# Kernel optimization log

Hardware: AMD Instinct MI355X
Metric: run time of the kernel (lower is better)

The kernel has to match this reference:

```python
import jax, jax.numpy as jnp
import numpy as np

NUM_ITEMS = 10000
EMBED_DIM = 64
USER_PERSPECTIVE_IMPORTANCE = 0.5
LEAKY_SLOPE = 0.2
BATCH = 32
MAX_HIST = 200


def setup_inputs() -> dict:
    key = jax.random.key(0)
    k_ids, k_len, k_items, k_user, k_w, k_b = jax.random.split(key, 6)
    batch_history_ids = jax.random.randint(k_ids, (BATCH, MAX_HIST), 0, NUM_ITEMS, dtype=jnp.int32)
    # lengths must be >= 1 to avoid all-masked softmax rows
    batch_history_lengths = jnp.maximum(
        jax.random.randint(k_len, (BATCH,), 0, MAX_HIST, dtype=jnp.int32), 1)
    items_embedding = jax.random.normal(k_items, (NUM_ITEMS, EMBED_DIM), dtype=jnp.float32)
    user_embedding = jax.random.normal(k_user, (1, EMBED_DIM), dtype=jnp.float32)
    fc_weight = jax.random.normal(k_w, (EMBED_DIM, EMBED_DIM), dtype=jnp.float32) * (1.0 / np.sqrt(EMBED_DIM))
    fc_bias = jax.random.normal(k_b, (EMBED_DIM,), dtype=jnp.float32) * 0.01
    return {
        'batch_history_ids': batch_history_ids,
        'batch_history_lengths': batch_history_lengths,
        'items_embedding': items_embedding,
        'user_embedding': user_embedding,
        'fc_weight': fc_weight,
        'fc_bias': fc_bias,
    }


def reference(batch_history_ids, batch_history_lengths, items_embedding, user_embedding, fc_weight, fc_bias):
    # valid[b, n] = n < length[b]
    valid = jnp.arange(MAX_HIST)[None, :] < batch_history_lengths[:, None]  # [B, N]

    hist_emb = items_embedding[batch_history_ids]  # [B, N, F] ragged gather (padded)

    # item-perspective attention: [B, I, N]
    item_att = jnp.einsum('if,bnf->bin', items_embedding, hist_emb)
    # original adds -inf mask then leaky_relu; leaky_relu(-inf) = -inf -> softmax weight 0
    item_att = jnp.where(valid[:, None, :], jax.nn.leaky_relu(item_att, LEAKY_SLOPE), -jnp.inf)
    item_scores = jax.nn.softmax(item_att, axis=-1)  # [B, I, N]

    # user-perspective attention: constant across the item-query axis (q=1, repeated over I),
    # so compute once as [B, N] and broadcast (same math as 'qif,bnf->bqin').
    user_att = jnp.einsum('f,bnf->bn', user_embedding[0], hist_emb)
    user_att = jnp.where(valid, jax.nn.leaky_relu(user_att, LEAKY_SLOPE), -jnp.inf)
    user_scores = jax.nn.softmax(user_att, axis=-1)  # [B, N]

    w = USER_PERSPECTIVE_IMPORTANCE
    attn = (1.0 - w) * item_scores + w * user_scores[:, None, :]  # [B, I, N]

    personalized = jnp.einsum('bin,bnf->bif', attn, hist_emb)  # [B, I, F]
    projected = personalized @ fc_weight.T + fc_bias  # [B, I, F]
    # final per-item score: dot with item embedding
    return jnp.einsum('bif,if->bi', projected, items_embedding)  # [B, I]
```

## Files before the change

### kernel.cpp

```cpp
#include <hip/hip_runtime.h>
#include <hip/hip_bf16.h>
#include <math.h>

#define NUM_ITEMS 10000
#define EMBED_DIM 64
#define MAX_HIST 200
#define NPAD 208
#define BATCH 32
#define LEAKY 0.2f
#define W_USER 0.5f
#define LOG2E 1.4426950408889634f
#define ECLAMP 110.0f
#define NWTI 157

typedef short bf16x8 __attribute__((ext_vector_type(8)));
typedef float f32x4 __attribute__((ext_vector_type(4)));

__device__ __forceinline__ unsigned short f2bf(float f) {
    __hip_bfloat16 h = __float2bfloat16(f);
    return __builtin_bit_cast(unsigned short, h);
}

__device__ __forceinline__ float bf2f(unsigned short u) {
    return __builtin_bit_cast(float, (unsigned int)u << 16);
}

__device__ __forceinline__ float fexp2(float x) {
#if __has_builtin(__builtin_amdgcn_exp2f)
    return __builtin_amdgcn_exp2f(x);
#else
    return exp2f(x);
#endif
}

__global__ __launch_bounds__(256) void prep_kernel(const int* __restrict__ ids,
                                                   const int* __restrict__ lens,
                                                   const float* __restrict__ items,
                                                   const float* __restrict__ user,
                                                   const float* __restrict__ W,
                                                   const float* __restrict__ bias,
                                                   unsigned short* __restrict__ items_att_bf,
                                                   unsigned short* __restrict__ wti_bf,
                                                   float* __restrict__ bdot,
                                                   unsigned short* __restrict__ hist_bf,
                                                   unsigned short* __restrict__ uh_bf) {
    const int tid = threadIdx.x;
    __shared__ __align__(16) char sbuf[NPAD * EMBED_DIM * 2];
    __shared__ float red[8];
    __shared__ float sh_usf[NPAD];
    __shared__ float sh_uh[4][EMBED_DIM];

    if (blockIdx.x < NWTI) {
        float* shW = (float*)sbuf;
        for (int idx = tid; idx < EMBED_DIM * EMBED_DIM; idx += 256) shW[idx] = W[idx];
        __syncthreads();

        const int g = tid & 63;
        const int isub = tid >> 6;
        const int base = blockIdx.x * 64 + isub * 16;

        for (int k = 0; k < 16; ++k) {
            const int i = base + k;
            if (i >= NUM_ITEMS) break;
            const float* irow = items + (size_t)i * EMBED_DIM;

            float acc = 0.f;
#pragma unroll
            for (int f = 0; f < EMBED_DIM; ++f) acc += irow[f] * shW[f * EMBED_DIM + g];

            wti_bf[i * EMBED_DIM + g] = f2bf(acc);
            items_att_bf[i * EMBED_DIM + g] = f2bf(irow[g] * LOG2E);

            float bv = bias[g] * irow[g];
#pragma unroll
            for (int o = 32; o > 0; o >>= 1) bv += __shfl_xor(bv, o, 64);
            if (g == 0) bdot[i] = bv;
        }
    } else {
        const int b = blockIdx.x - NWTI;
        unsigned short* sh_h = (unsigned short*)sbuf;

        for (int idx = tid; idx < NPAD * 8; idx += 256) {
            const int n = idx >> 3, q = idx & 7;
            bf16x8 v = (bf16x8)0;
            if (n < MAX_HIST) {
                const int id = ids[b * MAX_HIST + n];
                const float4* p = (const float4*)(items + id * EMBED_DIM + q * 8);
                float4 v0 = p[0], v1 = p[1];
                v[0] = (short)f2bf(v0.x); v[1] = (short)f2bf(v0.y);
                v[2] = (short)f2bf(v0.z); v[3] = (short)f2bf(v0.w);
                v[4] = (short)f2bf(v1.x); v[5] = (short)f2bf(v1.y);
                v[6] = (short)f2bf(v1.z); v[7] = (short)f2bf(v1.w);
            }
            *(bf16x8*)(hist_bf + (size_t)(b * NPAD + n) * EMBED_DIM + q * 8) = v;
            *(bf16x8*)(sh_h + (size_t)n * EMBED_DIM + q * 8) = v;
        }

        const int len = lens[b];
        float s = -INFINITY;
        if (tid < len) {
            const int id = ids[b * MAX_HIST + tid];
            const float* h = items + id * EMBED_DIM;
            float a0 = 0.f, a1 = 0.f;
#pragma unroll
            for (int f = 0; f < EMBED_DIM; f += 2) {
                a0 += user[f] * h[f];
                a1 += user[f + 1] * h[f + 1];
            }
            float a = a0 + a1;
            s = fmaxf(a, LEAKY * a);
        }
        float m = s;
#pragma unroll
        for (int o = 32; o > 0; o >>= 1) m = fmaxf(m, __shfl_xor(m, o, 64));
        if ((tid & 63) == 0) red[tid >> 6] = m;
        __syncthreads();
        m = fmaxf(fmaxf(red[0], red[1]), fmaxf(red[2], red[3]));

        float e = (tid < len) ? __expf(s - m) : 0.f;
        float t = e;
#pragma unroll
        for (int o = 32; o > 0; o >>= 1) t += __shfl_xor(t, o, 64);
        if ((tid & 63) == 0) red[4 + (tid >> 6)] = t;
        __syncthreads();
        const float sum = red[4] + red[5] + red[6] + red[7];

        if (tid < NPAD) sh_usf[tid] = (tid < len) ? (e / sum) : 0.f;
        __syncthreads();

        const int f = tid & 63;
        const int part = tid >> 6;
        float uhp = 0.f;
        for (int n = part; n < len; n += 4)
            uhp += sh_usf[n] * bf2f(sh_h[n * EMBED_DIM + f]);
        sh_uh[part][f] = uhp;
        __syncthreads();
        if (tid < EMBED_DIM)
            uh_bf[b * EMBED_DIM + tid] =
                f2bf(sh_uh[0][tid] + sh_uh[1][tid] + sh_uh[2][tid] + sh_uh[3][tid]);
    }
}

__global__ __launch_bounds__(256) void main_kernel(const unsigned short* __restrict__ items_att_bf,
                                                   const unsigned short* __restrict__ wti_bf,
                                                   const float* __restrict__ bdot,
                                                   const unsigned short* __restrict__ hist_bf,
                                                   const unsigned short* __restrict__ uh_bf,
                                                   const int* __restrict__ lens,
                                                   float* __restrict__ out) {
    const int b = blockIdx.y;
    const int tid = threadIdx.x;
    const int lane = tid & 63;
    const int w = tid >> 6;

    __shared__ __align__(16) unsigned short sh_hist[NPAD * EMBED_DIM];

    const int len = lens[b];
    const int ntiles = (len + 15) >> 4;

    const int c16 = lane & 15;
    const int g = lane >> 4;

    bf16x8 u0 = *(const bf16x8*)(uh_bf + b * 64 + g * 8);
    bf16x8 u1 = *(const bf16x8*)(uh_bf + b * 64 + 32 + g * 8);

    const float4* src = (const float4*)(hist_bf + (size_t)b * NPAD * EMBED_DIM);
    const int nf4 = ntiles * 16 * 8;
    for (int c = tid; c < nf4; c += 256) {
        const int n = c >> 3, q = c & 7;
        float4 v = src[c];
        const int byte = (n * 128 + q * 16) ^ ((n & 7) << 4);
        *(float4*)((char*)sh_hist + byte) = v;
    }
    __syncthreads();

    const char* hbase = (const char*)sh_hist;

#define LDA(T, X0, X1)                                                   \
    {                                                                    \
        const int n_ = (T) * 16 + c16;                                   \
        const int base_ = n_ * 128, sw_ = (n_ & 7) << 4;                 \
        X0 = *(const bf16x8*)(hbase + ((base_ + g * 16) ^ sw_));         \
        X1 = *(const bf16x8*)(hbase + ((base_ + 64 + g * 16) ^ sw_));    \
    }

#define EPI(S, H, Se, Sh, MASKED, NB)                                    \
    {                                                                    \
        float s0 = fminf(fmaxf(S[0], LEAKY * S[0]), ECLAMP);             \
        float s1 = fminf(fmaxf(S[1], LEAKY * S[1]), ECLAMP);             \
        float s2 = fminf(fmaxf(S[2], LEAKY * S[2]), ECLAMP);             \
        float s3 = fminf(fmaxf(S[3], LEAKY * S[3]), ECLAMP);             \
        if (MASKED) {                                                    \
            s0 = ((NB) + 0 < len) ? s0 : -INFINITY;                      \
            s1 = ((NB) + 1 < len) ? s1 : -INFINITY;                      \
            s2 = ((NB) + 2 < len) ? s2 : -INFINITY;                      \
            s3 = ((NB) + 3 < len) ? s3 : -INFINITY;                      \
        }                                                                \
        const float e0 = fexp2(s0), e1 = fexp2(s1);                      \
        const float e2 = fexp2(s2), e3 = fexp2(s3);                      \
        Se += (e0 + e1) + (e2 + e3);                                     \
        Sh = fmaf(e0, H[0], fmaf(e1, H[1], fmaf(e2, H[2], fmaf(e3, H[3], Sh)))); \
    }

    const int wbase = blockIdx.x * 256 + w * 16;

    int ild = min(wbase + c16, NUM_ITEMS - 1);
    bf16x8 itc0 = *(const bf16x8*)(items_att_bf + (size_t)ild * 64 + g * 8);
    bf16x8 itc1 = *(const bf16x8*)(items_att_bf + (size_t)ild * 64 + 32 + g * 8);
    bf16x8 wtc0 = *(const bf16x8*)(wti_bf + (size_t)ild * 64 + g * 8);
    bf16x8 wtc1 = *(const bf16x8*)(wti_bf + (size_t)ild * 64 + 32 + g * 8);

#pragma unroll
    for (int it = 0; it < 4; ++it) {
        const int gstart = wbase + it * 64;
        if (gstart >= NUM_ITEMS) break;

        bf16x8 nt0, nt1, nw0, nw1;
        if (it < 3) {
            const int inx = min(wbase + (it + 1) * 64 + c16, NUM_ITEMS - 1);
            nt0 = *(const bf16x8*)(items_att_bf + (size_t)inx * 64 + g * 8);
            nt1 = *(const bf16x8*)(items_att_bf + (size_t)inx * 64 + 32 + g * 8);
            nw0 = *(const bf16x8*)(wti_bf + (size_t)inx * 64 + g * 8);
            nw1 = *(const bf16x8*)(wti_bf + (size_t)inx * 64 + 32 + g * 8);
        }

        f32x4 suf = (f32x4)0.f;
        suf = __builtin_amdgcn_mfma_f32_16x16x32_bf16(u0, wtc0, suf, 0, 0, 0);
        suf = __builtin_amdgcn_mfma_f32_16x16x32_bf16(u1, wtc1, suf, 0, 0, 0);
        const float Su = suf[0];

        float Se = 0.f, Sh = 0.f;
        bf16x8 a0, a1;
        LDA(0, a0, a1)

        for (int t = 0; t < ntiles - 1; ++t) {
            f32x4 S = (f32x4)0.f, H = (f32x4)0.f;
            S = __builtin_amdgcn_mfma_f32_16x16x32_bf16(a0, itc0, S, 0, 0, 0);
            S = __builtin_amdgcn_mfma_f32_16x16x32_bf16(a1, itc1, S, 0, 0, 0);
            H = __builtin_amdgcn_mfma_f32_16x16x32_bf16(a0, wtc0, H, 0, 0, 0);
            H = __builtin_amdgcn_mfma_f32_16x16x32_bf16(a1, wtc1, H, 0, 0, 0);
            bf16x8 p0, p1;
            LDA(t + 1, p0, p1)
            EPI(S, H, Se, Sh, 0, 0)
            a0 = p0; a1 = p1;
        }
        {
            f32x4 S = (f32x4)0.f, H = (f32x4)0.f;
            S = __builtin_amdgcn_mfma_f32_16x16x32_bf16(a0, itc0, S, 0, 0, 0);
            S = __builtin_amdgcn_mfma_f32_16x16x32_bf16(a1, itc1, S, 0, 0, 0);
            H = __builtin_amdgcn_mfma_f32_16x16x32_bf16(a0, wtc0, H, 0, 0, 0);
            H = __builtin_amdgcn_mfma_f32_16x16x32_bf16(a1, wtc1, H, 0, 0, 0);
            const int nb = (ntiles - 1) * 16 + g * 4;
            EPI(S, H, Se, Sh, 1, nb)
        }

        Se += __shfl_xor(Se, 16, 64); Se += __shfl_xor(Se, 32, 64);
        Sh += __shfl_xor(Sh, 16, 64); Sh += __shfl_xor(Sh, 32, 64);

        if (g == 0) {
            const int i = gstart + c16;
            out[(size_t)b * NUM_ITEMS + i] =
                (1.0f - W_USER) * (Sh / Se) + W_USER * Su + bdot[i];
        }

        if (it < 3) { itc0 = nt0; itc1 = nt1; wtc0 = nw0; wtc1 = nw1; }
    }
#undef EPI
#undef LDA
}

extern "C" void kernel_launch(void* const* d_in, const int* in_sizes, int n_in,
                              void* d_out, int out_size, void* d_ws, size_t ws_size,
                              hipStream_t stream) {
    const int* ids = (const int*)d_in[0];
    const int* lens = (const int*)d_in[1];
    const float* items = (const float*)d_in[2];
    const float* user = (const float*)d_in[3];
    const float* W = (const float*)d_in[4];
    const float* bias = (const float*)d_in[5];
    float* out = (float*)d_out;

    char* p = (char*)d_ws;
    unsigned short* items_att_bf = (unsigned short*)p; p += (size_t)NUM_ITEMS * EMBED_DIM * 2;
    unsigned short* wti_bf       = (unsigned short*)p; p += (size_t)NUM_ITEMS * EMBED_DIM * 2;
    float* bdot                  = (float*)p;          p += (size_t)NUM_ITEMS * 4;
    unsigned short* hist_bf      = (unsigned short*)p; p += (size_t)BATCH * NPAD * EMBED_DIM * 2;
    unsigned short* uh_bf        = (unsigned short*)p; p += (size_t)BATCH * EMBED_DIM * 2;

    prep_kernel<<<NWTI + BATCH, 256, 0, stream>>>(ids, lens, items, user, W, bias,
                                                  items_att_bf, wti_bf, bdot,
                                                  hist_bf, uh_bf);

    dim3 grid((NUM_ITEMS + 255) / 256, BATCH);
    main_kernel<<<grid, 256, 0, stream>>>(items_att_bf, wti_bf, bdot, hist_bf, uh_bf, lens, out);
}
```

Measured before the change: 44.58 us.

## Apply FC weight to history side instead of items, using plain bf16 item cast

Reassociates the math so the fc_weight projection is applied to the per-batch history embeddings (histW = hist·Wᵀ, computed with MFMA in the prep kernel) and the log2e scale is folded into a second history copy. The user term and bias are also folded into a per-batch vector v, so the items side needs only a single bf16 cast. The main kernel then streams one item operand instead of two and drops the bdot lookup, at the cost of staging two history tiles in LDS and writing twice the history data in prep. The 64x64 per-item matvec in prep becomes a simple elementwise cast.

```diff
diff --git a/kernel.cpp b/kernel.cpp
--- a/kernel.cpp
+++ b/kernel.cpp
@@ -11,7 +11,7 @@
 #define W_USER 0.5f
 #define LOG2E 1.4426950408889634f
 #define ECLAMP 110.0f
-#define NWTI 157
+#define NCAST 313
 
 typedef short bf16x8 __attribute__((ext_vector_type(8)));
 typedef float f32x4 __attribute__((ext_vector_type(4)));
@@ -33,119 +33,148 @@
 #endif
 }
 
+__device__ __forceinline__ bf16x8 cvt8(float4 a, float4 b) {
+    bf16x8 v;
+    v[0] = (short)f2bf(a.x); v[1] = (short)f2bf(a.y);
+    v[2] = (short)f2bf(a.z); v[3] = (short)f2bf(a.w);
+    v[4] = (short)f2bf(b.x); v[5] = (short)f2bf(b.y);
+    v[6] = (short)f2bf(b.z); v[7] = (short)f2bf(b.w);
+    return v;
+}
+
 __global__ __launch_bounds__(256) void prep_kernel(const int* __restrict__ ids,
                                                    const int* __restrict__ lens,
                                                    const float* __restrict__ items,
                                                    const float* __restrict__ user,
                                                    const float* __restrict__ W,
                                                    const float* __restrict__ bias,
-                                                   unsigned short* __restrict__ items_att_bf,
-                                                   unsigned short* __restrict__ wti_bf,
-                                                   float* __restrict__ bdot,
-                                                   unsigned short* __restrict__ hist_bf,
-                                                   unsigned short* __restrict__ uh_bf) {
+                                                   unsigned short* __restrict__ items_bf,
+                                                   unsigned short* __restrict__ histL_bf,
+                                                   unsigned short* __restrict__ histW_bf,
+                                                   unsigned short* __restrict__ v_bf) {
     const int tid = threadIdx.x;
-    __shared__ __align__(16) char sbuf[NPAD * EMBED_DIM * 2];
+
+    if (blockIdx.x < NCAST) {
+        const int c = blockIdx.x * 256 + tid;
+        if (c < NUM_ITEMS * EMBED_DIM / 8) {
+            const float4* p = (const float4*)items + 2 * c;
+            *(bf16x8*)(items_bf + (size_t)c * 8) = cvt8(p[0], p[1]);
+        }
+        return;
+    }
+
+    const int b = blockIdx.x - NCAST;
+    __shared__ __align__(16) unsigned short sh_h[NPAD * EMBED_DIM];
     __shared__ float red[8];
     __shared__ float sh_usf[NPAD];
     __shared__ float sh_uh[4][EMBED_DIM];
-
-    if (blockIdx.x < NWTI) {
-        float* shW = (float*)sbuf;
-        for (int idx = tid; idx < EMBED_DIM * EMBED_DIM; idx += 256) shW[idx] = W[idx];
-        __syncthreads();
-
-        const int g = tid & 63;
-        const int isub = tid >> 6;
-        const int base = blockIdx.x * 64 + isub * 16;
-
-        for (int k = 0; k < 16; ++k) {
-            const int i = base + k;
-            if (i >= NUM_ITEMS) break;
-            const float* irow = items + (size_t)i * EMBED_DIM;
-
-            float acc = 0.f;
-#pragma unroll
-            for (int f = 0; f < EMBED_DIM; ++f) acc += irow[f] * shW[f * EMBED_DIM + g];
-
-            wti_bf[i * EMBED_DIM + g] = f2bf(acc);
-            items_att_bf[i * EMBED_DIM + g] = f2bf(irow[g] * LOG2E);
-
-            float bv = bias[g] * irow[g];
-#pragma unroll
-            for (int o = 32; o > 0; o >>= 1) bv += __shfl_xor(bv, o, 64);
-            if (g == 0) bdot[i] = bv;
-        }
-    } else {
-        const int b = blockIdx.x - NWTI;
-        unsigned short* sh_h = (unsigned short*)sbuf;
-
-        for (int idx = tid; idx < NPAD * 8; idx += 256) {
-            const int n = idx >> 3, q = idx & 7;
-            bf16x8 v = (bf16x8)0;
-            if (n < MAX_HIST) {
-                const int id = ids[b * MAX_HIST + n];
-                const float4* p = (const float4*)(items + id * EMBED_DIM + q * 8);
-                float4 v0 = p[0], v1 = p[1];
-                v[0] = (short)f2bf(v0.x); v[1] = (short)f2bf(v0.y);
-                v[2] = (short)f2bf(v0.z); v[3] = (short)f2bf(v0.w);
-                v[4] = (short)f2bf(v1.x); v[5] = (short)f2bf(v1.y);
-                v[6] = (short)f2bf(v1.z); v[7] = (short)f2bf(v1.w);
+    __shared__ float sh_uhf[EMBED_DIM];
+
+    const int len = lens[b];
+    const int ntiles = (len + 15) >> 4;
+
+    for (int idx = tid; idx < NPAD * 8; idx += 256) {
+        const int n = idx >> 3;
+        bf16x8 vu = (bf16x8)0, vs = (bf16x8)0;
+        if (n < MAX_HIST) {
+            const int id = ids[b * MAX_HIST + n];
+            const float4* p = (const float4*)(items + (size_t)id * EMBED_DIM + (idx & 7) * 8);
+            float4 v0 = p[0], v1 = p[1];
+            vu = cvt8(v0, v1);
+            float4 s0 = make_float4(v0.x * LOG2E, v0.y * LOG2E, v0.z * LOG2E, v0.w * LOG2E);
+            float4 s1 = make_float4(v1.x * LOG2E, v1.y * LOG2E, v1.z * LOG2E, v1.w * LOG2E);
+            vs = cvt8(s0, s1);
+        }
+        *(bf16x8*)(sh_h + (size_t)idx * 8) = vu;
+        *(bf16x8*)(histL_bf + (size_t)b * NPAD * EMBED_DIM + (size_t)idx * 8) = vs;
+    }
+    __syncthreads();
+
+    {
+        const int lane = tid & 63;
+        const int w = tid >> 6;
+        const int c16 = lane & 15;
+        const int g = lane >> 4;
+        const int f = w * 16 + c16;
+        const float* wrow = W + (size_t)f * EMBED_DIM;
+        float4 wa = *(const float4*)(wrow + g * 8);
+        float4 wb = *(const float4*)(wrow + g * 8 + 4);
+        float4 wc = *(const float4*)(wrow + 32 + g * 8);
+        float4 wd = *(const float4*)(wrow + 32 + g * 8 + 4);
+        bf16x8 b0 = cvt8(wa, wb), b1 = cvt8(wc, wd);
+
+        for (int t = 0; t < ntiles; ++t) {
+            const int n = t * 16 + c16;
+            bf16x8 a0 = *(const bf16x8*)(sh_h + n * EMBED_DIM + g * 8);
+            bf16x8 a1 = *(const bf16x8*)(sh_h + n * EMBED_DIM + 32 + g * 8);
+            f32x4 D = (f32x4)0.f;
+            D = __builtin_amdgcn_mfma_f32_16x16x32_bf16(a0, b0, D, 0, 0, 0);
+            D = __builtin_amdgcn_mfma_f32_16x16x32_bf16(a1, b1, D, 0, 0, 0);
+#pragma unroll
+            for (int j = 0; j < 4; ++j) {
+                const int nr = t * 16 + g * 4 + j;
+                histW_bf[(size_t)(b * NPAD + nr) * EMBED_DIM + f] = f2bf(D[j]);
             }
-            *(bf16x8*)(hist_bf + (size_t)(b * NPAD + n) * EMBED_DIM + q * 8) = v;
-            *(bf16x8*)(sh_h + (size_t)n * EMBED_DIM + q * 8) = v;
-        }
-
-        const int len = lens[b];
-        float s = -INFINITY;
-        if (tid < len) {
-            const int id = ids[b * MAX_HIST + tid];
-            const float* h = items + id * EMBED_DIM;
-            float a0 = 0.f, a1 = 0.f;
-#pragma unroll
-            for (int f = 0; f < EMBED_DIM; f += 2) {
-                a0 += user[f] * h[f];
-                a1 += user[f + 1] * h[f + 1];
-            }
-            float a = a0 + a1;
-            s = fmaxf(a, LEAKY * a);
-        }
-        float m = s;
-#pragma unroll
-        for (int o = 32; o > 0; o >>= 1) m = fmaxf(m, __shfl_xor(m, o, 64));
-        if ((tid & 63) == 0) red[tid >> 6] = m;
-        __syncthreads();
-        m = fmaxf(fmaxf(red[0], red[1]), fmaxf(red[2], red[3]));
-
-        float e = (tid < len) ? __expf(s - m) : 0.f;
-        float t = e;
-#pragma unroll
-        for (int o = 32; o > 0; o >>= 1) t += __shfl_xor(t, o, 64);
-        if ((tid & 63) == 0) red[4 + (tid >> 6)] = t;
-        __syncthreads();
-        const float sum = red[4] + red[5] + red[6] + red[7];
-
-        if (tid < NPAD) sh_usf[tid] = (tid < len) ? (e / sum) : 0.f;
-        __syncthreads();
-
+        }
+    }
+
+    float s = -INFINITY;
+    if (tid < len) {
+        const int id = ids[b * MAX_HIST + tid];
+        const float* h = items + (size_t)id * EMBED_DIM;
+        float a0 = 0.f, a1 = 0.f;
+#pragma unroll
+        for (int fi = 0; fi < EMBED_DIM; fi += 2) {
+            a0 += user[fi] * h[fi];
+            a1 += user[fi + 1] * h[fi + 1];
+        }
+        float a = a0 + a1;
+        s = fmaxf(a, LEAKY * a);
+    }
+    float m = s;
+#pragma unroll
+    for (int o = 32; o > 0; o >>= 1) m = fmaxf(m, __shfl_xor(m, o, 64));
+    if ((tid & 63) == 0) red[tid >> 6] = m;
+    __syncthreads();
+    m = fmaxf(fmaxf(red[0], red[1]), fmaxf(red[2], red[3]));
+
+    float e = (tid < len) ? __expf(s - m) : 0.f;
+    float t = e;
+#pragma unroll
+    for (int o = 32; o > 0; o >>= 1) t += __shfl_xor(t, o, 64);
+    if ((tid & 63) == 0) red[4 + (tid >> 6)] = t;
+    __syncthreads();
+    const float sum = red[4] + red[5] + red[6] + red[7];
+
+    if (tid < NPAD) sh_usf[tid] = (tid < len) ? (e / sum) : 0.f;
+    __syncthreads();
+
+    {
         const int f = tid & 63;
         const int part = tid >> 6;
         float uhp = 0.f;
         for (int n = part; n < len; n += 4)
             uhp += sh_usf[n] * bf2f(sh_h[n * EMBED_DIM + f]);
         sh_uh[part][f] = uhp;
-        __syncthreads();
-        if (tid < EMBED_DIM)
-            uh_bf[b * EMBED_DIM + tid] =
-                f2bf(sh_uh[0][tid] + sh_uh[1][tid] + sh_uh[2][tid] + sh_uh[3][tid]);
-    }
-}
-
-__global__ __launch_bounds__(256) void main_kernel(const unsigned short* __restrict__ items_att_bf,
-                                                   const unsigned short* __restrict__ wti_bf,
-                                                   const float* __restrict__ bdot,
-                                                   const unsigned short* __restrict__ hist_bf,
-                                                   const unsigned short* __restrict__ uh_bf,
+    }
+    __syncthreads();
+    if (tid < EMBED_DIM)
+        sh_uhf[tid] = sh_uh[0][tid] + sh_uh[1][tid] + sh_uh[2][tid] + sh_uh[3][tid];
+    __syncthreads();
+
+    if (tid < EMBED_DIM) {
+        const float* wrow = W + (size_t)tid * EMBED_DIM;
+        float acc = 0.f;
+#pragma unroll 8
+        for (int g2 = 0; g2 < EMBED_DIM; ++g2) acc += sh_uhf[g2] * wrow[g2];
+        v_bf[b * EMBED_DIM + tid] = f2bf(W_USER * acc + bias[tid]);
+    }
+}
+
+__global__ __launch_bounds__(256) void main_kernel(const unsigned short* __restrict__ items_bf,
+                                                   const unsigned short* __restrict__ histL_bf,
+                                                   const unsigned short* __restrict__ histW_bf,
+                                                   const unsigned short* __restrict__ v_bf,
                                                    const int* __restrict__ lens,
                                                    float* __restrict__ out) {
     const int b = blockIdx.y;
@@ -153,7 +182,8 @@
     const int lane = tid & 63;
     const int w = tid >> 6;
 
-    __shared__ __align__(16) unsigned short sh_hist[NPAD * EMBED_DIM];
+    __shared__ __align__(16) unsigned short sh_L[NPAD * EMBED_DIM];
+    __shared__ __align__(16) unsigned short sh_W[NPAD * EMBED_DIM];
 
     const int len = lens[b];
     const int ntiles = (len + 15) >> 4;
@@ -161,27 +191,28 @@
     const int c16 = lane & 15;
     const int g = lane >> 4;
 
-    bf16x8 u0 = *(const bf16x8*)(uh_bf + b * 64 + g * 8);
-    bf16x8 u1 = *(const bf16x8*)(uh_bf + b * 64 + 32 + g * 8);
-
-    const float4* src = (const float4*)(hist_bf + (size_t)b * NPAD * EMBED_DIM);
+    bf16x8 v0 = *(const bf16x8*)(v_bf + b * 64 + g * 8);
+    bf16x8 v1 = *(const bf16x8*)(v_bf + b * 64 + 32 + g * 8);
+
     const int nf4 = ntiles * 16 * 8;
-    for (int c = tid; c < nf4; c += 256) {
-        const int n = c >> 3, q = c & 7;
-        float4 v = src[c];
-        const int byte = (n * 128 + q * 16) ^ ((n & 7) << 4);
-        *(float4*)((char*)sh_hist + byte) = v;
-    }
-    __syncthreads();
-
-    const char* hbase = (const char*)sh_hist;
-
-#define LDA(T, X0, X1)                                                   \
-    {                                                                    \
-        const int n_ = (T) * 16 + c16;                                   \
-        const int base_ = n_ * 128, sw_ = (n_ & 7) << 4;                 \
-        X0 = *(const bf16x8*)(hbase + ((base_ + g * 16) ^ sw_));         \
-        X1 = *(const bf16x8*)(hbase + ((base_ + 64 + g * 16) ^ sw_));    \
+    {
+        const float4* srcL = (const float4*)(histL_bf + (size_t)b * NPAD * EMBED_DIM);
+        const float4* srcW = (const float4*)(histW_bf + (size_t)b * NPAD * EMBED_DIM);
+        for (int c = tid; c < nf4; c += 256) {
+            const int n = c >> 3, q = c & 7;
+            const int byte = (n * 128 + q * 16) ^ ((n & 7) << 4);
+            *(float4*)((char*)sh_L + byte) = srcL[c];
+            *(float4*)((char*)sh_W + byte) = srcW[c];
+        }
+    }
+    __syncthreads();
+
+#define LDA(BASE, T, X0, X1)                                                  \
+    {                                                                         \
+        const int n_ = (T) * 16 + c16;                                        \
+        const int base_ = n_ * 128, sw_ = (n_ & 7) << 4;                      \
+        X0 = *(const bf16x8*)((const char*)(BASE) + ((base_ + g * 16) ^ sw_));\
+        X1 = *(const bf16x8*)((const char*)(BASE) + ((base_ + 64 + g * 16) ^ sw_)); \
     }
 
 #define EPI(S, H, Se, Sh, MASKED, NB)                                    \
@@ -205,51 +236,49 @@
     const int wbase = blockIdx.x * 256 + w * 16;
 
     int ild = min(wbase + c16, NUM_ITEMS - 1);
-    bf16x8 itc0 = *(const bf16x8*)(items_att_bf + (size_t)ild * 64 + g * 8);
-    bf16x8 itc1 = *(const bf16x8*)(items_att_bf + (size_t)ild * 64 + 32 + g * 8);
-    bf16x8 wtc0 = *(const bf16x8*)(wti_bf + (size_t)ild * 64 + g * 8);
-    bf16x8 wtc1 = *(const bf16x8*)(wti_bf + (size_t)ild * 64 + 32 + g * 8);
+    bf16x8 itc0 = *(const bf16x8*)(items_bf + (size_t)ild * 64 + g * 8);
+    bf16x8 itc1 = *(const bf16x8*)(items_bf + (size_t)ild * 64 + 32 + g * 8);
 
 #pragma unroll
     for (int it = 0; it < 4; ++it) {
         const int gstart = wbase + it * 64;
         if (gstart >= NUM_ITEMS) break;
 
-        bf16x8 nt0, nt1, nw0, nw1;
+        bf16x8 nt0, nt1;
         if (it < 3) {
             const int inx = min(wbase + (it + 1) * 64 + c16, NUM_ITEMS - 1);
-            nt0 = *(const bf16x8*)(items_att_bf + (size_t)inx * 64 + g * 8);
-            nt1 = *(const bf16x8*)(items_att_bf + (size_t)inx * 64 + 32 + g * 8);
-            nw0 = *(const bf16x8*)(wti_bf + (size_t)inx * 64 + g * 8);
-            nw1 = *(const bf16x8*)(wti_bf + (size_t)inx * 64 + 32 + g * 8);
+            nt0 = *(const bf16x8*)(items_bf + (size_t)inx * 64 + g * 8);
+            nt1 = *(const bf16x8*)(items_bf + (size_t)inx * 64 + 32 + g * 8);
         }
 
         f32x4 suf = (f32x4)0.f;
-        suf = __builtin_amdgcn_mfma_f32_16x16x32_bf16(u0, wtc0, suf, 0, 0, 0);
-        suf = __builtin_amdgcn_mfma_f32_16x16x32_bf16(u1, wtc1, suf, 0, 0, 0);
-        const float Su = suf[0];
+        suf = __builtin_amdgcn_mfma_f32_16x16x32_bf16(v0, itc0, suf, 0, 0, 0);
+        suf = __builtin_amdgcn_mfma_f32_16x16x32_bf16(v1, itc1, suf, 0, 0, 0);
+        const float Sv = suf[0];
 
         float Se = 0.f, Sh = 0.f;
-        bf16x8 a0, a1;
-        LDA(0, a0, a1)
+        bf16x8 aL0, aL1, aW0, aW1;
+        LDA(sh_L, 0, aL0, aL1)
+        LDA(sh_W, 0, aW0, aW1)
 
         for (int t = 0; t < ntiles - 1; ++t) {
             f32x4 S = (f32x4)0.f, H = (f32x4)0.f;
-            S = __builtin_amdgcn_mfma_f32_16x16x32_bf16(a0, itc0, S, 0, 0, 0);
-            S = __builtin_amdgcn_mfma_f32_16x16x32_bf16(a1, itc1, S, 0, 0, 0);
-            H = __builtin_amdgcn_mfma_f32_16x16x32_bf16(a0, wtc0, H, 0, 0, 0);
-            H = __builtin_amdgcn_mfma_f32_16x16x32_bf16(a1, wtc1, H, 0, 0, 0);
-            bf16x8 p0, p1;
-            LDA(t + 1, p0, p1)
+            S = __builtin_amdgcn_mfma_f32_16x16x32_bf16(aL0, itc0, S, 0, 0, 0);
+            S = __builtin_amdgcn_mfma_f32_16x16x32_bf16(aL1, itc1, S, 0, 0, 0);
+            H = __builtin_amdgcn_mfma_f32_16x16x32_bf16(aW0, itc0, H, 0, 0, 0);
+            H = __builtin_amdgcn_mfma_f32_16x16x32_bf16(aW1, itc1, H, 0, 0, 0);
+            bf16x8 pL0, pL1, pW0, pW1;
+            LDA(sh_L, t + 1, pL0, pL1)
+            LDA(sh_W, t + 1, pW0, pW1)
             EPI(S, H, Se, Sh, 0, 0)
-            a0 = p0; a1 = p1;
+            aL0 = pL0; aL1 = pL1; aW0 = pW0; aW1 = pW1;
         }
         {
             f32x4 S = (f32x4)0.f, H = (f32x4)0.f;
-            S = __builtin_amdgcn_mfma_f32_16x16x32_bf16(a0, itc0, S, 0, 0, 0);
-            S = __builtin_amdgcn_mfma_f32_16x16x32_bf16(a1, itc1, S, 0, 0, 0);
-            H = __builtin_amdgcn_mfma_f32_16x16x32_bf16(a0, wtc0, H, 0, 0, 0);
-            H = __builtin_amdgcn_mfma_f32_16x16x32_bf16(a1, wtc1, H, 0, 0, 0);
+            S = __builtin_amdgcn_mfma_f32_16x16x32_bf16(aL0, itc0, S, 0, 0, 0);
+            S = __builtin_amdgcn_mfma_f32_16x16x32_bf16(aL1, itc1, S, 0, 0, 0);
+            H = __builtin_amdgcn_mfma_f32_16x16x32_bf16(aW0, itc0, H, 0, 0, 0);
+            H = __builtin_amdgcn_mfma_f32_16x16x32_bf16(aW1, itc1, H, 0, 0, 0);
             const int nb = (ntiles - 1) * 16 + g * 4;
             EPI(S, H, Se, Sh, 1, nb)
         }
@@ -259,11 +288,10 @@
 
         if (g == 0) {
             const int i = gstart + c16;
-            out[(size_t)b * NUM_ITEMS + i] =
-                (1.0f - W_USER) * (Sh / Se) + W_USER * Su + bdot[i];
-        }
-
-        if (it < 3) { itc0 = nt0; itc1 = nt1; wtc0 = nw0; wtc1 = nw1; }
+            out[(size_t)b * NUM_ITEMS + i] = (1.0f - W_USER) * (Sh / Se) + Sv;
+        }
+
+        if (it < 3) { itc0 = nt0; itc1 = nt1; }
     }
 #undef EPI
 #undef LDA
@@ -281,16 +309,14 @@
     float* out = (float*)d_out;
 
     char* p = (char*)d_ws;
-    unsigned short* items_att_bf = (unsigned short*)p; p += (size_t)NUM_ITEMS * EMBED_DIM * 2;
-    unsigned short* wti_bf       = (unsigned short*)p; p += (size_t)NUM_ITEMS * EMBED_DIM * 2;
-    float* bdot                  = (float*)p;          p += (size_t)NUM_ITEMS * 4;
-    unsigned short* hist_bf      = (unsigned short*)p; p += (size_t)BATCH * NPAD * EMBED_DIM * 2;
-    unsigned short* uh_bf        = (unsigned short*)p; p += (size_t)BATCH * EMBED_DIM * 2;
-
-    prep_kernel<<<NWTI + BATCH, 256, 0, stream>>>(ids, lens, items, user, W, bias,
-                                                  items_att_bf, wti_bf, bdot,
-                                                  hist_bf, uh_bf);
+    unsigned short* items_bf = (unsigned short*)p; p += (size_t)NUM_ITEMS * EMBED_DIM * 2;
+    unsigned short* histL_bf = (unsigned short*)p; p += (size_t)BATCH * NPAD * EMBED_DIM * 2;
+    unsigned short* histW_bf = (unsigned short*)p; p += (size_t)BATCH * NPAD * EMBED_DIM * 2;
+    unsigned short* v_bf     = (unsigned short*)p; p += (size_t)BATCH * EMBED_DIM * 2;
+
+    prep_kernel<<<NCAST + BATCH, 256, 0, stream>>>(ids, lens, items, user, W, bias,
+                                                   items_bf, histL_bf, histW_bf, v_bf);
 
     dim3 grid((NUM_ITEMS + 255) / 256, BATCH);
-    main_kernel<<<grid, 256, 0, stream>>>(items_att_bf, wti_bf, bdot, hist_bf, uh_bf, lens, out);
-}
+    main_kernel<<<grid, 256, 0, stream>>>(items_bf, histL_bf, histW_bf, v_bf, lens, out);
+}
```

Measured after the change: 41.11 us. -7.8%, faster.
